# Kernel tuning notes

Hardware: AMD Instinct MI355X
Metric: run time of the kernel (lower is better)

## Reference

```python
import jax, jax.numpy as jnp
import numpy as np

HOPS = 3  # C[i].weight tied to A[i+1].weight -> HOPS+1 distinct tables E_0..E_HOPS


def setup_inputs() -> dict:
    key = jax.random.key(0)
    ks = jax.random.split(key, 10)
    B, M, K, E, G, V = 32, 2048, 4, 128, 128, 50000
    s = 1.0 / np.sqrt(E).astype(np.float32)
    context = jax.random.randint(ks[0], (B, M, K), 0, V)          # memory (triples)
    h_ = jax.random.normal(ks[1], (B, G), dtype=jnp.float32)      # prev GRU hidden
    y_ = jax.random.randint(ks[2], (B,), 0, V)                    # prev token
    emb = jax.random.normal(ks[3], (HOPS + 1, V, E), dtype=jnp.float32) * 0.1
    W_ih = jax.random.normal(ks[4], (3 * G, E), dtype=jnp.float32) * s
    W_hh = jax.random.normal(ks[5], (3 * G, G), dtype=jnp.float32) * s
    b_ih = jax.random.normal(ks[6], (3 * G,), dtype=jnp.float32) * s
    b_hh = jax.random.normal(ks[7], (3 * G,), dtype=jnp.float32) * s
    W_vocab = jax.random.normal(ks[8], (V, 2 * E), dtype=jnp.float32) * s
    b_vocab = jax.random.normal(ks[9], (V,), dtype=jnp.float32) * s
    return dict(context=context, h_=h_, y_=y_, emb=emb, W_ih=W_ih, W_hh=W_hh,
                b_ih=b_ih, b_hh=b_hh, W_vocab=W_vocab, b_vocab=b_vocab)


def gru_cell(x, h, W_ih, W_hh, b_ih, b_hh):
    # PyTorch GRU cell semantics (r, z, n gate order).
    gi = x @ W_ih.T + b_ih
    gh = h @ W_hh.T + b_hh
    i_r, i_z, i_n = jnp.split(gi, 3, axis=-1)
    h_r, h_z, h_n = jnp.split(gh, 3, axis=-1)
    r = jax.nn.sigmoid(i_r + h_r)
    z = jax.nn.sigmoid(i_z + h_z)
    n = jnp.tanh(i_n + r * h_n)
    return (1.0 - z) * n + z * h


def reference(context, h_, y_, emb, W_ih, W_hh, b_ih, b_hh, W_vocab, b_vocab):
    x = emb[0][y_]                                   # [B, E] A[0] embed of prev token
    h = gru_cell(x, h_, W_ih, W_hh, b_ih, b_hh)      # [B, G], G == E
    q = h
    o1 = None
    attn = None
    for hop in range(HOPS):
        mA = emb[hop][context].sum(axis=2)           # gather [B,M,K,E] -> sum over K -> [B,M,E]
        p = jnp.einsum('bme,be->bm', mA, q)          # attention scores over memory slots
        attn = jax.nn.softmax(p, axis=1)             # [B, M]
        mC = emb[hop + 1][context].sum(axis=2)       # C[hop] table (tied to A[hop+1])
        o = jnp.einsum('bm,bme->be', attn, mC)       # memory read [B, E]
        q = q + o
        if hop == 0:
            o1 = o
    logits = jnp.concatenate([h, o1], axis=1) @ W_vocab.T + b_vocab  # [B, V]
    p_vocab = jax.nn.softmax(logits, axis=1)
    return h, p_vocab, attn
```

## Files before the change

kernel.cpp:

```cpp
#include <hip/hip_runtime.h>
#include <math.h>

#define BB 32
#define MM 2048
#define KK 4
#define EE 128
#define GG 128
#define VV 50000
#define HOPS 3

__global__ __launch_bounds__(384) void gru_kernel(
    const float* __restrict__ emb0,
    const int*   __restrict__ y,
    const float* __restrict__ hprev,
    const float* __restrict__ W_ih,
    const float* __restrict__ W_hh,
    const float* __restrict__ b_ih,
    const float* __restrict__ b_hh,
    float* __restrict__ h_out,
    float* __restrict__ q)
{
    int b = blockIdx.x;
    int t = threadIdx.x;
    __shared__ float x[EE], h[GG], gi[3*GG], gh[3*GG];
    if (t < EE)            x[t]       = emb0[(size_t)y[b]*EE + t];
    else if (t < 2*EE)     h[t-EE]    = hprev[b*GG + (t-EE)];
    __syncthreads();
    {
        float accI = b_ih[t], accH = b_hh[t];
        const float* wi = W_ih + (size_t)t*EE;
        const float* wh = W_hh + (size_t)t*GG;
        #pragma unroll 8
        for (int e = 0; e < EE; e++) { accI += x[e]*wi[e]; accH += h[e]*wh[e]; }
        gi[t] = accI; gh[t] = accH;
    }
    __syncthreads();
    if (t < GG) {
        float r = 1.f/(1.f + __expf(-(gi[t]        + gh[t])));
        float z = 1.f/(1.f + __expf(-(gi[GG+t]     + gh[GG+t])));
        float n = tanhf(gi[2*GG+t] + r*gh[2*GG+t]);
        float hn = (1.f - z)*n + z*h[t];
        h_out[b*GG + t] = hn;
        q[b*GG + t]     = hn;
    }
}

__global__ __launch_bounds__(256) void scores_kernel(
    const float* __restrict__ embT,
    const int*   __restrict__ ctx,
    const float* __restrict__ q,
    float* __restrict__ p)
{
    int gid  = blockIdx.x * 4 + (threadIdx.x >> 6);
    int lane = threadIdx.x & 63;
    int b    = gid >> 11;
    const int4 c = *(const int4*)(ctx + (size_t)gid*KK);
    float2 qv = *(const float2*)(q + b*EE + lane*2);
    float2 v0 = *(const float2*)(embT + (size_t)c.x*EE + lane*2);
    float2 v1 = *(const float2*)(embT + (size_t)c.y*EE + lane*2);
    float2 v2 = *(const float2*)(embT + (size_t)c.z*EE + lane*2);
    float2 v3 = *(const float2*)(embT + (size_t)c.w*EE + lane*2);
    float sx = v0.x + v1.x + v2.x + v3.x;
    float sy = v0.y + v1.y + v2.y + v3.y;
    float acc = sx*qv.x + sy*qv.y;
    #pragma unroll
    for (int off = 32; off; off >>= 1) acc += __shfl_down(acc, off);
    if (lane == 0) p[gid] = acc;
}

__global__ __launch_bounds__(256) void softmax_m_kernel(
    const float* __restrict__ p,
    float* __restrict__ attn)
{
    int b = blockIdx.x, t = threadIdx.x;
    const float* row = p + (size_t)b*MM;
    float v[8];
    float mx = -INFINITY;
    #pragma unroll
    for (int i = 0; i < 8; i++) { v[i] = row[t + i*256]; mx = fmaxf(mx, v[i]); }
    __shared__ float red[6];
    int w = t >> 6, lane = t & 63;
    #pragma unroll
    for (int off = 32; off; off >>= 1) mx = fmaxf(mx, __shfl_down(mx, off));
    if (lane == 0) red[w] = mx;
    __syncthreads();
    if (t == 0) { float m2 = fmaxf(fmaxf(red[0],red[1]), fmaxf(red[2],red[3])); red[4] = m2; }
    __syncthreads();
    mx = red[4];
    float sum = 0.f;
    #pragma unroll
    for (int i = 0; i < 8; i++) { v[i] = __expf(v[i] - mx); sum += v[i]; }
    #pragma unroll
    for (int off = 32; off; off >>= 1) sum += __shfl_down(sum, off);
    if (lane == 0) red[w] = sum;
    __syncthreads();
    if (t == 0) { red[5] = 1.f / (red[0]+red[1]+red[2]+red[3]); }
    __syncthreads();
    float rs = red[5];
    #pragma unroll
    for (int i = 0; i < 8; i++) attn[(size_t)b*MM + t + i*256] = v[i]*rs;
}

__global__ __launch_bounds__(256) void oacc_kernel(
    const float* __restrict__ embT,
    const int*   __restrict__ ctx,
    const float* __restrict__ attn,
    float* __restrict__ o_part)
{
    int blk = blockIdx.x;
    int b = blk >> 5, s = blk & 31;
    int w = threadIdx.x >> 6, lane = threadIdx.x & 63;
    int m0 = s*64 + w*16;
    float ax = 0.f, ay = 0.f;
    for (int i = 0; i < 16; i++) {
        int m = m0 + i;
        float a = attn[(size_t)b*MM + m];
        const int4 c = *(const int4*)(ctx + (size_t)(b*MM + m)*KK);
        float2 v0 = *(const float2*)(embT + (size_t)c.x*EE + lane*2);
        float2 v1 = *(const float2*)(embT + (size_t)c.y*EE + lane*2);
        float2 v2 = *(const float2*)(embT + (size_t)c.z*EE + lane*2);
        float2 v3 = *(const float2*)(embT + (size_t)c.w*EE + lane*2);
        ax += a * (v0.x + v1.x + v2.x + v3.x);
        ay += a * (v0.y + v1.y + v2.y + v3.y);
    }
    __shared__ float red[4][EE];
    red[w][lane*2]   = ax;
    red[w][lane*2+1] = ay;
    __syncthreads();
    if (threadIdx.x < EE) {
        int e = threadIdx.x;
        float v = red[0][e] + red[1][e] + red[2][e] + red[3][e];
        o_part[((size_t)s*BB + b)*EE + e] = v;
    }
}

__global__ __launch_bounds__(256) void qupd_kernel(
    const float* __restrict__ o_part,
    float* __restrict__ q,
    float* __restrict__ o1,
    int save_o1)
{
    int i = blockIdx.x*256 + threadIdx.x;
    float v = 0.f;
    #pragma unroll 8
    for (int s = 0; s < 32; s++) v += o_part[(size_t)s*BB*EE + i];
    q[i] += v;
    if (save_o1) o1[i] = v;
}

__global__ __launch_bounds__(256) void logits_kernel(
    const float* __restrict__ h,
    const float* __restrict__ o1,
    const float* __restrict__ Wv,
    const float* __restrict__ bv,
    float* __restrict__ logits)
{
    __shared__ float Ut[256][32];
    __shared__ float Wt[32][132];
    int t = threadIdx.x;
    for (int i = t; i < 256*32; i += 256) {
        int e = i >> 5, b = i & 31;
        Ut[e][b] = (e < GG) ? h[b*GG + e] : o1[b*EE + (e - GG)];
    }
    int vg = t & 31;
    int bg = t >> 5;
    int v0 = blockIdx.x * 128;
    float acc[4][4];
    #pragma unroll
    for (int i = 0; i < 4; i++)
        #pragma unroll
        for (int j = 0; j < 4; j++) acc[i][j] = 0.f;

    int vrow = t >> 1;
    int half = t & 1;
    const float* wrow = Wv + (size_t)(v0 + vrow)*256 + half*16;
    bool vok = (v0 + vrow) < VV;

    for (int ec = 0; ec < 256; ec += 32) {
        __syncthreads();
        #pragma unroll
        for (int j = 0; j < 4; j++) {
            float4 w = make_float4(0.f, 0.f, 0.f, 0.f);
            if (vok) w = *(const float4*)(wrow + ec + j*4);
            int e0 = half*16 + j*4;
            Wt[e0+0][vrow] = w.x;
            Wt[e0+1][vrow] = w.y;
            Wt[e0+2][vrow] = w.z;
            Wt[e0+3][vrow] = w.w;
        }
        __syncthreads();
        #pragma unroll 8
        for (int e = 0; e < 32; e++) {
            float4 w = *(const float4*)(&Wt[e][vg*4]);
            float4 u = *(const float4*)(&Ut[ec + e][bg*4]);
            acc[0][0] += w.x*u.x; acc[0][1] += w.x*u.y; acc[0][2] += w.x*u.z; acc[0][3] += w.x*u.w;
            acc[1][0] += w.y*u.x; acc[1][1] += w.y*u.y; acc[1][2] += w.y*u.z; acc[1][3] += w.y*u.w;
            acc[2][0] += w.z*u.x; acc[2][1] += w.z*u.y; acc[2][2] += w.z*u.z; acc[2][3] += w.z*u.w;
            acc[3][0] += w.w*u.x; acc[3][1] += w.w*u.y; acc[3][2] += w.w*u.z; acc[3][3] += w.w*u.w;
        }
    }
    #pragma unroll
    for (int i = 0; i < 4; i++) {
        int v = v0 + vg*4 + i;
        if (v < VV) {
            float bb = bv[v];
            #pragma unroll
            for (int j = 0; j < 4; j++)
                logits[(size_t)(bg*4 + j)*VV + v] = acc[i][j] + bb;
        }
    }
}

#define VCHUNK 6250
__global__ __launch_bounds__(256) void vpart_kernel(
    const float* __restrict__ logits,
    float* __restrict__ part)
{
    int blk = blockIdx.x;
    int b = blk >> 3, c = blk & 7;
    int t = threadIdx.x;
    const float* row = logits + (size_t)b*VV;
    int start = c*VCHUNK;
    int end   = min(start + VCHUNK, VV);
    __shared__ float red[4];
    int w = t >> 6, lane = t & 63;
    float mx = -INFINITY;
    for (int i = start + t; i < end; i += 256) mx = fmaxf(mx, row[i]);
    #pragma unroll
    for (int off = 32; off; off >>= 1) mx = fmaxf(mx, __shfl_down(mx, off));
    if (lane == 0) red[w] = mx;
    __syncthreads();
    float m = fmaxf(fmaxf(red[0], red[1]), fmaxf(red[2], red[3]));
    float sum = 0.f;
    for (int i = start + t; i < end; i += 256) sum += __expf(row[i] - m);
    #pragma unroll
    for (int off = 32; off; off >>= 1) sum += __shfl_down(sum, off);
    __syncthreads();
    if (lane == 0) red[w] = sum;
    __syncthreads();
    if (t == 0) {
        part[blk*2]   = m;
        part[blk*2+1] = red[0] + red[1] + red[2] + red[3];
    }
}

__global__ __launch_bounds__(256) void vfinal_kernel(
    float* __restrict__ logits,
    const float* __restrict__ part)
{
    int i = blockIdx.x*256 + threadIdx.x;
    if (i >= BB*VV) return;
    int b = i / VV;
    const float* pp = part + b*16;
    float M = -INFINITY;
    #pragma unroll
    for (int c = 0; c < 8; c++) M = fmaxf(M, pp[c*2]);
    float S = 0.f;
    #pragma unroll
    for (int c = 0; c < 8; c++) S += pp[c*2+1] * __expf(pp[c*2] - M);
    logits[i] = __expf(logits[i] - M) * (1.f / S);
}

extern "C" void kernel_launch(void* const* d_in, const int* in_sizes, int n_in,
                              void* d_out, int out_size, void* d_ws, size_t ws_size,
                              hipStream_t stream) {
    const int*   ctx    = (const int*)  d_in[0];
    const float* h_prev = (const float*)d_in[1];
    const int*   y      = (const int*)  d_in[2];
    const float* emb    = (const float*)d_in[3];
    const float* W_ih   = (const float*)d_in[4];
    const float* W_hh   = (const float*)d_in[5];
    const float* b_ih   = (const float*)d_in[6];
    const float* b_hh   = (const float*)d_in[7];
    const float* Wv     = (const float*)d_in[8];
    const float* bv     = (const float*)d_in[9];

    float* out_h    = (float*)d_out;
    float* out_pv   = out_h + BB*GG;
    float* out_attn = out_pv + (size_t)BB*VV;

    float* ws     = (float*)d_ws;
    float* q      = ws;
    float* o1     = q + BB*EE;
    float* o_part = o1 + BB*EE;
    float* p      = o_part + 32*BB*EE;
    float* attn   = p + BB*MM;
    float* part   = attn + BB*MM;

    gru_kernel<<<BB, 384, 0, stream>>>(emb, y, h_prev, W_ih, W_hh, b_ih, b_hh, out_h, q);

    for (int hop = 0; hop < HOPS; hop++) {
        const float* embA = emb + (size_t)hop*VV*EE;
        const float* embC = emb + (size_t)(hop+1)*VV*EE;
        scores_kernel<<<(BB*MM)/4, 256, 0, stream>>>(embA, ctx, q, p);
        float* attn_dst = (hop == HOPS-1) ? out_attn : attn;
        softmax_m_kernel<<<BB, 256, 0, stream>>>(p, attn_dst);
        oacc_kernel<<<BB*32, 256, 0, stream>>>(embC, ctx, attn_dst, o_part);
        qupd_kernel<<<(BB*EE)/256, 256, 0, stream>>>(o_part, q, o1, hop == 0 ? 1 : 0);
    }

    logits_kernel<<<(VV + 127)/128, 256, 0, stream>>>(out_h, o1, Wv, bv, out_pv);
    vpart_kernel<<<BB*8, 256, 0, stream>>>(out_pv, part);
    vfinal_kernel<<<(BB*VV + 255)/256, 256, 0, stream>>>(out_pv, part);
}
```

Measured before the change: 359.8 us.

## Fuse pipeline into cooperative megakernels and compute scores via q·E table GEMM

The many small launches are replaced by two cooperative persistent kernels that use grid-wide syncs. Attention scores are now computed by a dense GEMM of q against each whole embedding table, followed by a gather-sum of the per-token dot products. This replaces gathering 128-wide rows per memory slot. Softmax normalisation is folded into the read-out pass, the q and o1 updates use atomics, and the vocab softmax runs one block per row. In exchange the score step reads the full 50000x128 table for each hop, there are grid syncs, and results become nondeterministic because of the atomics.

```diff
diff --git a/kernel.cpp b/kernel.cpp
--- a/kernel.cpp
+++ b/kernel.cpp
@@ -1,5 +1,8 @@
 #include <hip/hip_runtime.h>
+#include <hip/hip_cooperative_groups.h>
 #include <math.h>
+
+namespace cg = cooperative_groups;
 
 #define BB 32
 #define MM 2048
@@ -7,258 +10,287 @@
 #define EE 128
 #define GG 128
 #define VV 50000
-#define HOPS 3
-
-__global__ __launch_bounds__(384) void gru_kernel(
-    const float* __restrict__ emb0,
+#define NT1 391
+#define NBLK 1024
+
+__global__ __launch_bounds__(256, 4) void mega1(
+    const int*   __restrict__ ctx,
     const int*   __restrict__ y,
     const float* __restrict__ hprev,
-    const float* __restrict__ W_ih,
-    const float* __restrict__ W_hh,
-    const float* __restrict__ b_ih,
-    const float* __restrict__ b_hh,
+    const float* __restrict__ emb,
+    const float* __restrict__ W_ih, const float* __restrict__ W_hh,
+    const float* __restrict__ b_ih, const float* __restrict__ b_hh,
     float* __restrict__ h_out,
-    float* __restrict__ q)
-{
-    int b = blockIdx.x;
-    int t = threadIdx.x;
-    __shared__ float x[EE], h[GG], gi[3*GG], gh[3*GG];
-    if (t < EE)            x[t]       = emb0[(size_t)y[b]*EE + t];
-    else if (t < 2*EE)     h[t-EE]    = hprev[b*GG + (t-EE)];
-    __syncthreads();
-    {
-        float accI = b_ih[t], accH = b_hh[t];
-        const float* wi = W_ih + (size_t)t*EE;
-        const float* wh = W_hh + (size_t)t*GG;
-        #pragma unroll 8
-        for (int e = 0; e < EE; e++) { accI += x[e]*wi[e]; accH += h[e]*wh[e]; }
-        gi[t] = accI; gh[t] = accH;
-    }
-    __syncthreads();
-    if (t < GG) {
-        float r = 1.f/(1.f + __expf(-(gi[t]        + gh[t])));
-        float z = 1.f/(1.f + __expf(-(gi[GG+t]     + gh[GG+t])));
-        float n = tanhf(gi[2*GG+t] + r*gh[2*GG+t]);
-        float hn = (1.f - z)*n + z*h[t];
-        h_out[b*GG + t] = hn;
-        q[b*GG + t]     = hn;
-    }
-}
-
-__global__ __launch_bounds__(256) void scores_kernel(
-    const float* __restrict__ embT,
-    const int*   __restrict__ ctx,
-    const float* __restrict__ q,
-    float* __restrict__ p)
-{
-    int gid  = blockIdx.x * 4 + (threadIdx.x >> 6);
-    int lane = threadIdx.x & 63;
-    int b    = gid >> 11;
-    const int4 c = *(const int4*)(ctx + (size_t)gid*KK);
-    float2 qv = *(const float2*)(q + b*EE + lane*2);
-    float2 v0 = *(const float2*)(embT + (size_t)c.x*EE + lane*2);
-    float2 v1 = *(const float2*)(embT + (size_t)c.y*EE + lane*2);
-    float2 v2 = *(const float2*)(embT + (size_t)c.z*EE + lane*2);
-    float2 v3 = *(const float2*)(embT + (size_t)c.w*EE + lane*2);
-    float sx = v0.x + v1.x + v2.x + v3.x;
-    float sy = v0.y + v1.y + v2.y + v3.y;
-    float acc = sx*qv.x + sy*qv.y;
-    #pragma unroll
-    for (int off = 32; off; off >>= 1) acc += __shfl_down(acc, off);
-    if (lane == 0) p[gid] = acc;
-}
-
-__global__ __launch_bounds__(256) void softmax_m_kernel(
-    const float* __restrict__ p,
-    float* __restrict__ attn)
-{
-    int b = blockIdx.x, t = threadIdx.x;
-    const float* row = p + (size_t)b*MM;
-    float v[8];
-    float mx = -INFINITY;
-    #pragma unroll
-    for (int i = 0; i < 8; i++) { v[i] = row[t + i*256]; mx = fmaxf(mx, v[i]); }
-    __shared__ float red[6];
-    int w = t >> 6, lane = t & 63;
-    #pragma unroll
-    for (int off = 32; off; off >>= 1) mx = fmaxf(mx, __shfl_down(mx, off));
-    if (lane == 0) red[w] = mx;
-    __syncthreads();
-    if (t == 0) { float m2 = fmaxf(fmaxf(red[0],red[1]), fmaxf(red[2],red[3])); red[4] = m2; }
-    __syncthreads();
-    mx = red[4];
-    float sum = 0.f;
-    #pragma unroll
-    for (int i = 0; i < 8; i++) { v[i] = __expf(v[i] - mx); sum += v[i]; }
-    #pragma unroll
-    for (int off = 32; off; off >>= 1) sum += __shfl_down(sum, off);
-    if (lane == 0) red[w] = sum;
-    __syncthreads();
-    if (t == 0) { red[5] = 1.f / (red[0]+red[1]+red[2]+red[3]); }
-    __syncthreads();
-    float rs = red[5];
-    #pragma unroll
-    for (int i = 0; i < 8; i++) attn[(size_t)b*MM + t + i*256] = v[i]*rs;
-}
-
-__global__ __launch_bounds__(256) void oacc_kernel(
-    const float* __restrict__ embT,
-    const int*   __restrict__ ctx,
-    const float* __restrict__ attn,
-    float* __restrict__ o_part)
-{
-    int blk = blockIdx.x;
-    int b = blk >> 5, s = blk & 31;
-    int w = threadIdx.x >> 6, lane = threadIdx.x & 63;
-    int m0 = s*64 + w*16;
-    float ax = 0.f, ay = 0.f;
-    for (int i = 0; i < 16; i++) {
-        int m = m0 + i;
-        float a = attn[(size_t)b*MM + m];
-        const int4 c = *(const int4*)(ctx + (size_t)(b*MM + m)*KK);
-        float2 v0 = *(const float2*)(embT + (size_t)c.x*EE + lane*2);
-        float2 v1 = *(const float2*)(embT + (size_t)c.y*EE + lane*2);
-        float2 v2 = *(const float2*)(embT + (size_t)c.z*EE + lane*2);
-        float2 v3 = *(const float2*)(embT + (size_t)c.w*EE + lane*2);
-        ax += a * (v0.x + v1.x + v2.x + v3.x);
-        ay += a * (v0.y + v1.y + v2.y + v3.y);
-    }
-    __shared__ float red[4][EE];
-    red[w][lane*2]   = ax;
-    red[w][lane*2+1] = ay;
-    __syncthreads();
-    if (threadIdx.x < EE) {
-        int e = threadIdx.x;
-        float v = red[0][e] + red[1][e] + red[2][e] + red[3][e];
-        o_part[((size_t)s*BB + b)*EE + e] = v;
-    }
-}
-
-__global__ __launch_bounds__(256) void qupd_kernel(
-    const float* __restrict__ o_part,
+    float* __restrict__ attn_out,
     float* __restrict__ q,
     float* __restrict__ o1,
-    int save_o1)
+    float* __restrict__ tbuf,
+    float* __restrict__ p,
+    float* __restrict__ spart)
 {
-    int i = blockIdx.x*256 + threadIdx.x;
-    float v = 0.f;
-    #pragma unroll 8
-    for (int s = 0; s < 32; s++) v += o_part[(size_t)s*BB*EE + i];
-    q[i] += v;
-    if (save_o1) o1[i] = v;
+    cg::grid_group grid = cg::this_grid();
+    __shared__ float shraw[8320];
+    float* Ut = shraw;
+    float* Wt = shraw + 4096;
+    float* gx  = shraw;
+    float* ghh = shraw + 128;
+    float* ggi = shraw + 256;
+    float* ggh = shraw + 640;
+    float* sp   = shraw;
+    float* accr = shraw + 64;
+
+    int bid = blockIdx.x, tid = threadIdx.x, gsz = gridDim.x;
+
+    for (int b = bid; b < BB; b += gsz) {
+        if (tid < EE)      gx[tid] = emb[(size_t)y[b]*EE + tid];
+        else               ghh[tid-EE] = hprev[b*GG + (tid-EE)];
+        if (tid < EE)      o1[b*EE + tid] = 0.f;
+        __syncthreads();
+        for (int r = tid; r < 3*GG; r += 256) {
+            float accI = b_ih[r], accH = b_hh[r];
+            const float* wi = W_ih + (size_t)r*EE;
+            const float* wh = W_hh + (size_t)r*GG;
+            #pragma unroll 8
+            for (int e = 0; e < EE; e++) { accI += gx[e]*wi[e]; accH += ghh[e]*wh[e]; }
+            ggi[r] = accI; ggh[r] = accH;
+        }
+        __syncthreads();
+        if (tid < GG) {
+            float r_ = 1.f/(1.f + __expf(-(ggi[tid]      + ggh[tid])));
+            float z  = 1.f/(1.f + __expf(-(ggi[GG+tid]   + ggh[GG+tid])));
+            float n  = tanhf(ggi[2*GG+tid] + r_*ggh[2*GG+tid]);
+            float hn = (1.f - z)*n + z*ghh[tid];
+            h_out[b*GG + tid] = hn;
+            q[b*GG + tid]     = hn;
+        }
+        __syncthreads();
+    }
+    grid.sync();
+
+    for (int h = 0; h < 3; h++) {
+        const float* embA = emb + (size_t)h*VV*EE;
+
+        for (int tile = bid; tile < NT1; tile += gsz) {
+            __syncthreads();
+            for (int i = tid; i < EE*32; i += 256)
+                Ut[i] = q[(size_t)(i & 31)*EE + (i >> 5)];
+            int vg = tid & 31, bg = tid >> 5;
+            int v0 = tile * 128;
+            float acc[4][4];
+            #pragma unroll
+            for (int i = 0; i < 4; i++)
+                #pragma unroll
+                for (int j = 0; j < 4; j++) acc[i][j] = 0.f;
+            int vrow = tid >> 1, half = tid & 1;
+            const float* wrow = embA + (size_t)(v0 + vrow)*EE + half*16;
+            bool vok = (v0 + vrow) < VV;
+            for (int ec = 0; ec < EE; ec += 32) {
+                __syncthreads();
+                #pragma unroll
+                for (int j = 0; j < 4; j++) {
+                    float4 w = make_float4(0.f,0.f,0.f,0.f);
+                    if (vok) w = *(const float4*)(wrow + ec + j*4);
+                    int e0 = half*16 + j*4;
+                    Wt[(e0+0)*132 + vrow] = w.x;
+                    Wt[(e0+1)*132 + vrow] = w.y;
+                    Wt[(e0+2)*132 + vrow] = w.z;
+                    Wt[(e0+3)*132 + vrow] = w.w;
+                }
+                __syncthreads();
+                #pragma unroll 8
+                for (int e = 0; e < 32; e++) {
+                    float4 w = *(const float4*)(&Wt[e*132 + vg*4]);
+                    float4 u = *(const float4*)(&Ut[(ec + e)*32 + bg*4]);
+                    acc[0][0] += w.x*u.x; acc[0][1] += w.x*u.y; acc[0][2] += w.x*u.z; acc[0][3] += w.x*u.w;
+                    acc[1][0] += w.y*u.x; acc[1][1] += w.y*u.y; acc[1][2] += w.y*u.z; acc[1][3] += w.y*u.w;
+                    acc[2][0] += w.z*u.x; acc[2][1] += w.z*u.y; acc[2][2] += w.z*u.z; acc[2][3] += w.z*u.w;
+                    acc[3][0] += w.w*u.x; acc[3][1] += w.w*u.y; acc[3][2] += w.w*u.z; acc[3][3] += w.w*u.w;
+                }
+            }
+            #pragma unroll
+            for (int i = 0; i < 4; i++) {
+                int v = v0 + vg*4 + i;
+                if (v < VV) {
+                    #pragma unroll
+                    for (int j = 0; j < 4; j++)
+                        tbuf[(size_t)(bg*4 + j)*VV + v] = acc[i][j];
+                }
+            }
+        }
+        grid.sync();
+
+        for (int blk = bid; blk < NBLK; blk += gsz) {
+            int b = blk >> 5, s = blk & 31, m0 = s*64;
+            int j = tid >> 2, k = tid & 3;
+            int m = m0 + j;
+            int cidx = ctx[(((size_t)b << 11) + m)*KK + k];
+            float val = tbuf[(size_t)b*VV + cidx];
+            val += __shfl_down(val, 2);
+            val += __shfl_down(val, 1);
+            __syncthreads();
+            if ((tid & 3) == 0) { sp[j] = val; p[((size_t)b << 11) + m] = val; }
+            __syncthreads();
+            if (tid < 64) {
+                float v1 = sp[tid];
+                float m1 = v1;
+                #pragma unroll
+                for (int off = 32; off; off >>= 1) m1 = fmaxf(m1, __shfl_down(m1, off));
+                m1 = __shfl(m1, 0);
+                float s1 = __expf(v1 - m1);
+                #pragma unroll
+                for (int off = 32; off; off >>= 1) s1 += __shfl_down(s1, off);
+                if (tid == 0)
+                    *(float2*)(spart + ((size_t)b*32 + s)*2) = make_float2(m1, s1);
+            }
+        }
+        grid.sync();
+
+        if (h < 2) {
+            const float* embC = emb + (size_t)(h+1)*VV*EE;
+            for (int blk = bid; blk < NBLK; blk += gsz) {
+                int b = blk >> 5, s = blk & 31;
+                float M = -INFINITY;
+                for (int i2 = 0; i2 < 32; i2++)
+                    M = fmaxf(M, spart[((size_t)b*32 + i2)*2]);
+                float Z = 0.f;
+                for (int i2 = 0; i2 < 32; i2++) {
+                    float2 pr = *(const float2*)(spart + ((size_t)b*32 + i2)*2);
+                    Z += __expf(pr.x - M) * pr.y;
+                }
+                float invZ = 1.f / Z;
+                int w = tid >> 6, lane = tid & 63;
+                int m0 = s*64 + w*16;
+                float ax = 0.f, ay = 0.f;
+                for (int i = 0; i < 16; i++) {
+                    int m = m0 + i;
+                    float a = __expf(p[((size_t)b << 11) + m] - M) * invZ;
+                    const int4 c = *(const int4*)(ctx + (((size_t)b << 11) + m)*KK);
+                    float2 v0 = *(const float2*)(embC + (size_t)c.x*EE + lane*2);
+                    float2 v1 = *(const float2*)(embC + (size_t)c.y*EE + lane*2);
+                    float2 v2 = *(const float2*)(embC + (size_t)c.z*EE + lane*2);
+                    float2 v3 = *(const float2*)(embC + (size_t)c.w*EE + lane*2);
+                    ax += a * (v0.x + v1.x + v2.x + v3.x);
+                    ay += a * (v0.y + v1.y + v2.y + v3.y);
+                }
+                __syncthreads();
+                accr[w*EE + lane*2]     = ax;
+                accr[w*EE + lane*2 + 1] = ay;
+                __syncthreads();
+                if (tid < EE) {
+                    float vv = accr[tid] + accr[EE+tid] + accr[2*EE+tid] + accr[3*EE+tid];
+                    atomicAdd(&q[b*EE + tid], vv);
+                    if (h == 0) atomicAdd(&o1[b*EE + tid], vv);
+                }
+            }
+        } else {
+            for (int blk = bid; blk < NBLK; blk += gsz) {
+                int b = blk >> 5, s = blk & 31;
+                float M = -INFINITY;
+                for (int i2 = 0; i2 < 32; i2++)
+                    M = fmaxf(M, spart[((size_t)b*32 + i2)*2]);
+                float Z = 0.f;
+                for (int i2 = 0; i2 < 32; i2++) {
+                    float2 pr = *(const float2*)(spart + ((size_t)b*32 + i2)*2);
+                    Z += __expf(pr.x - M) * pr.y;
+                }
+                float invZ = 1.f / Z;
+                if (tid < 64) {
+                    int m = s*64 + tid;
+                    attn_out[((size_t)b << 11) + m] =
+                        __expf(p[((size_t)b << 11) + m] - M) * invZ;
+                }
+            }
+        }
+        grid.sync();
+    }
 }
 
-__global__ __launch_bounds__(256) void logits_kernel(
+__global__ __launch_bounds__(256, 3) void mega2(
     const float* __restrict__ h,
     const float* __restrict__ o1,
     const float* __restrict__ Wv,
     const float* __restrict__ bv,
     float* __restrict__ logits)
 {
-    __shared__ float Ut[256][32];
-    __shared__ float Wt[32][132];
-    int t = threadIdx.x;
-    for (int i = t; i < 256*32; i += 256) {
-        int e = i >> 5, b = i & 31;
-        Ut[e][b] = (e < GG) ? h[b*GG + e] : o1[b*EE + (e - GG)];
-    }
-    int vg = t & 31;
-    int bg = t >> 5;
-    int v0 = blockIdx.x * 128;
-    float acc[4][4];
-    #pragma unroll
-    for (int i = 0; i < 4; i++)
+    cg::grid_group grid = cg::this_grid();
+    __shared__ float Ut[256*32];
+    __shared__ float Wt[32*132];
+    __shared__ float red[8];
+    int tid = threadIdx.x, bid = blockIdx.x, gsz = gridDim.x;
+
+    for (int tile = bid; tile < NT1; tile += gsz) {
+        __syncthreads();
+        for (int i = tid; i < 256*32; i += 256) {
+            int e = i >> 5, b = i & 31;
+            Ut[i] = (e < GG) ? h[b*GG + e] : o1[b*EE + (e - GG)];
+        }
+        int vg = tid & 31, bg = tid >> 5;
+        int v0 = tile * 128;
+        float acc[4][4];
         #pragma unroll
-        for (int j = 0; j < 4; j++) acc[i][j] = 0.f;
-
-    int vrow = t >> 1;
-    int half = t & 1;
-    const float* wrow = Wv + (size_t)(v0 + vrow)*256 + half*16;
-    bool vok = (v0 + vrow) < VV;
-
-    for (int ec = 0; ec < 256; ec += 32) {
-        __syncthreads();
+        for (int i = 0; i < 4; i++)
+            #pragma unroll
+            for (int j = 0; j < 4; j++) acc[i][j] = 0.f;
+        int vrow = tid >> 1, half = tid & 1;
+        const float* wrow = Wv + (size_t)(v0 + vrow)*256 + half*16;
+        bool vok = (v0 + vrow) < VV;
+        for (int ec = 0; ec < 256; ec += 32) {
+            __syncthreads();
+            #pragma unroll
+            for (int j = 0; j < 4; j++) {
+                float4 w = make_float4(0.f,0.f,0.f,0.f);
+                if (vok) w = *(const float4*)(wrow + ec + j*4);
+                int e0 = half*16 + j*4;
+                Wt[(e0+0)*132 + vrow] = w.x;
+                Wt[(e0+1)*132 + vrow] = w.y;
+                Wt[(e0+2)*132 + vrow] = w.z;
+                Wt[(e0+3)*132 + vrow] = w.w;
+            }
+            __syncthreads();
+            #pragma unroll 8
+            for (int e = 0; e < 32; e++) {
+                float4 w = *(const float4*)(&Wt[e*132 + vg*4]);
+                float4 u = *(const float4*)(&Ut[(ec + e)*32 + bg*4]);
+                acc[0][0] += w.x*u.x; acc[0][1] += w.x*u.y; acc[0][2] += w.x*u.z; acc[0][3] += w.x*u.w;
+                acc[1][0] += w.y*u.x; acc[1][1] += w.y*u.y; acc[1][2] += w.y*u.z; acc[1][3] += w.y*u.w;
+                acc[2][0] += w.z*u.x; acc[2][1] += w.z*u.y; acc[2][2] += w.z*u.z; acc[2][3] += w.z*u.w;
+                acc[3][0] += w.w*u.x; acc[3][1] += w.w*u.y; acc[3][2] += w.w*u.z; acc[3][3] += w.w*u.w;
+            }
+        }
         #pragma unroll
-        for (int j = 0; j < 4; j++) {
-            float4 w = make_float4(0.f, 0.f, 0.f, 0.f);
-            if (vok) w = *(const float4*)(wrow + ec + j*4);
-            int e0 = half*16 + j*4;
-            Wt[e0+0][vrow] = w.x;
-            Wt[e0+1][vrow] = w.y;
-            Wt[e0+2][vrow] = w.z;
-            Wt[e0+3][vrow] = w.w;
-        }
-        __syncthreads();
-        #pragma unroll 8
-        for (int e = 0; e < 32; e++) {
-            float4 w = *(const float4*)(&Wt[e][vg*4]);
-            float4 u = *(const float4*)(&Ut[ec + e][bg*4]);
-            acc[0][0] += w.x*u.x; acc[0][1] += w.x*u.y; acc[0][2] += w.x*u.z; acc[0][3] += w.x*u.w;
-            acc[1][0] += w.y*u.x; acc[1][1] += w.y*u.y; acc[1][2] += w.y*u.z; acc[1][3] += w.y*u.w;
-            acc[2][0] += w.z*u.x; acc[2][1] += w.z*u.y; acc[2][2] += w.z*u.z; acc[2][3] += w.z*u.w;
-            acc[3][0] += w.w*u.x; acc[3][1] += w.w*u.y; acc[3][2] += w.w*u.z; acc[3][3] += w.w*u.w;
-        }
-    }
-    #pragma unroll
-    for (int i = 0; i < 4; i++) {
-        int v = v0 + vg*4 + i;
-        if (v < VV) {
-            float bb = bv[v];
-            #pragma unroll
-            for (int j = 0; j < 4; j++)
-                logits[(size_t)(bg*4 + j)*VV + v] = acc[i][j] + bb;
-        }
-    }
-}
-
-#define VCHUNK 6250
-__global__ __launch_bounds__(256) void vpart_kernel(
-    const float* __restrict__ logits,
-    float* __restrict__ part)
-{
-    int blk = blockIdx.x;
-    int b = blk >> 3, c = blk & 7;
-    int t = threadIdx.x;
-    const float* row = logits + (size_t)b*VV;
-    int start = c*VCHUNK;
-    int end   = min(start + VCHUNK, VV);
-    __shared__ float red[4];
-    int w = t >> 6, lane = t & 63;
-    float mx = -INFINITY;
-    for (int i = start + t; i < end; i += 256) mx = fmaxf(mx, row[i]);
-    #pragma unroll
-    for (int off = 32; off; off >>= 1) mx = fmaxf(mx, __shfl_down(mx, off));
-    if (lane == 0) red[w] = mx;
-    __syncthreads();
-    float m = fmaxf(fmaxf(red[0], red[1]), fmaxf(red[2], red[3]));
-    float sum = 0.f;
-    for (int i = start + t; i < end; i += 256) sum += __expf(row[i] - m);
-    #pragma unroll
-    for (int off = 32; off; off >>= 1) sum += __shfl_down(sum, off);
-    __syncthreads();
-    if (lane == 0) red[w] = sum;
-    __syncthreads();
-    if (t == 0) {
-        part[blk*2]   = m;
-        part[blk*2+1] = red[0] + red[1] + red[2] + red[3];
-    }
-}
-
-__global__ __launch_bounds__(256) void vfinal_kernel(
-    float* __restrict__ logits,
-    const float* __restrict__ part)
-{
-    int i = blockIdx.x*256 + threadIdx.x;
-    if (i >= BB*VV) return;
-    int b = i / VV;
-    const float* pp = part + b*16;
-    float M = -INFINITY;
-    #pragma unroll
-    for (int c = 0; c < 8; c++) M = fmaxf(M, pp[c*2]);
-    float S = 0.f;
-    #pragma unroll
-    for (int c = 0; c < 8; c++) S += pp[c*2+1] * __expf(pp[c*2] - M);
-    logits[i] = __expf(logits[i] - M) * (1.f / S);
+        for (int i = 0; i < 4; i++) {
+            int v = v0 + vg*4 + i;
+            if (v < VV) {
+                float bb = bv[v];
+                #pragma unroll
+                for (int j = 0; j < 4; j++)
+                    logits[(size_t)(bg*4 + j)*VV + v] = acc[i][j] + bb;
+            }
+        }
+    }
+    grid.sync();
+
+    for (int b = bid; b < BB; b += gsz) {
+        float* row = logits + (size_t)b*VV;
+        int w = tid >> 6, lane = tid & 63;
+        float mx = -INFINITY;
+        for (int i = tid; i < VV; i += 256) mx = fmaxf(mx, row[i]);
+        #pragma unroll
+        for (int off = 32; off; off >>= 1) mx = fmaxf(mx, __shfl_down(mx, off));
+        if (lane == 0) red[w] = mx;
+        __syncthreads();
+        float M = fmaxf(fmaxf(red[0], red[1]), fmaxf(red[2], red[3]));
+        float s = 0.f;
+        for (int i = tid; i < VV; i += 256) s += __expf(row[i] - M);
+        #pragma unroll
+        for (int off = 32; off; off >>= 1) s += __shfl_down(s, off);
+        __syncthreads();
+        if (lane == 0) red[w] = s;
+        __syncthreads();
+        float invS = 1.f / (red[0] + red[1] + red[2] + red[3]);
+        for (int i = tid; i < VV; i += 256) row[i] = __expf(row[i] - M) * invS;
+        __syncthreads();
+    }
 }
 
 extern "C" void kernel_launch(void* const* d_in, const int* in_sizes, int n_in,
@@ -279,27 +311,39 @@
     float* out_pv   = out_h + BB*GG;
     float* out_attn = out_pv + (size_t)BB*VV;
 
-    float* ws     = (float*)d_ws;
-    float* q      = ws;
-    float* o1     = q + BB*EE;
-    float* o_part = o1 + BB*EE;
-    float* p      = o_part + 32*BB*EE;
-    float* attn   = p + BB*MM;
-    float* part   = attn + BB*MM;
-
-    gru_kernel<<<BB, 384, 0, stream>>>(emb, y, h_prev, W_ih, W_hh, b_ih, b_hh, out_h, q);
-
-    for (int hop = 0; hop < HOPS; hop++) {
-        const float* embA = emb + (size_t)hop*VV*EE;
-        const float* embC = emb + (size_t)(hop+1)*VV*EE;
-        scores_kernel<<<(BB*MM)/4, 256, 0, stream>>>(embA, ctx, q, p);
-        float* attn_dst = (hop == HOPS-1) ? out_attn : attn;
-        softmax_m_kernel<<<BB, 256, 0, stream>>>(p, attn_dst);
-        oacc_kernel<<<BB*32, 256, 0, stream>>>(embC, ctx, attn_dst, o_part);
-        qupd_kernel<<<(BB*EE)/256, 256, 0, stream>>>(o_part, q, o1, hop == 0 ? 1 : 0);
-    }
-
-    logits_kernel<<<(VV + 127)/128, 256, 0, stream>>>(out_h, o1, Wv, bv, out_pv);
-    vpart_kernel<<<BB*8, 256, 0, stream>>>(out_pv, part);
-    vfinal_kernel<<<(BB*VV + 255)/256, 256, 0, stream>>>(out_pv, part);
+    float* ws    = (float*)d_ws;
+    float* q     = ws;
+    float* o1    = q + BB*EE;
+    float* p     = o1 + BB*EE;
+    float* tbuf  = p + BB*MM;
+    float* spart = tbuf + (size_t)BB*VV;
+
+    static int g1 = 0, g2 = 0;
+    if (g1 == 0) {
+        int mb = 0;
+        if (hipOccupancyMaxActiveBlocksPerMultiprocessor(
+                &mb, reinterpret_cast<const void*>(mega1), 256, 0) == hipSuccess && mb > 0)
+            g1 = mb * 256;
+        else
+            g1 = 4 * 256;
+        if (g1 > NBLK) g1 = NBLK;
+        mb = 0;
+        if (hipOccupancyMaxActiveBlocksPerMultiprocessor(
+                &mb, reinterpret_cast<const void*>(mega2), 256, 0) == hipSuccess && mb > 0)
+            g2 = mb * 256;
+        else
+            g2 = 3 * 256;
+        if (g2 > NT1) g2 = NT1;
+    }
+
+    void* a1[] = { (void*)&ctx, (void*)&y, (void*)&h_prev, (void*)&emb,
+                   (void*)&W_ih, (void*)&W_hh, (void*)&b_ih, (void*)&b_hh,
+                   (void*)&out_h, (void*)&out_attn,
+                   (void*)&q, (void*)&o1, (void*)&tbuf, (void*)&p, (void*)&spart };
+    hipLaunchCooperativeKernel(reinterpret_cast<const void*>(mega1),
+                               dim3(g1), dim3(256), a1, 0, stream);
+
+    void* a2[] = { (void*)&out_h, (void*)&o1, (void*)&Wv, (void*)&bv, (void*)&out_pv };
+    hipLaunchCooperativeKernel(reinterpret_cast<const void*>(mega2),
+                               dim3(g2), dim3(256), a2, 0, stream);
 }
```

Result: slower. 1.046 ms (+190.7%).
